# Performance work log

Hardware: AMD Instinct MI355X
Metric: run time of the kernel (lower is better)

Reference implementation:

```python
import jax, jax.numpy as jnp
import numpy as np

NUM_HEADS = 16
TOP_K = 2

def setup_inputs() -> dict:
    key = jax.random.key(0)
    ks = jax.random.split(key, 5)
    B, D, E = 8192, 2048, 8
    x = jax.random.normal(ks[0], (B, D), dtype=jnp.float32)
    W_qkv = jax.random.normal(ks[1], (E, D, 3 * D), dtype=jnp.float32) * 0.02  # (in,out) per expert
    W_gate = jax.random.normal(ks[2], (D, E), dtype=jnp.float32) * 0.02
    b_gate = jnp.zeros((E,), dtype=jnp.float32)
    W_proj = jax.random.normal(ks[3], (D, D), dtype=jnp.float32) * 0.02
    b_proj = jnp.zeros((D,), dtype=jnp.float32)
    return {"x": x, "W_qkv": W_qkv, "W_gate": W_gate, "b_gate": b_gate,
            "W_proj": W_proj, "b_proj": b_proj}


def reference(x, W_qkv, W_gate, b_gate, W_proj, b_proj):
    B, D = x.shape
    E = W_qkv.shape[0]
    H = NUM_HEADS
    hd = D // H
    scale = float(hd) ** -0.5

    # gating + top-k (sparse gate weights, zeros for non-selected experts)
    gate_scores = jax.nn.softmax(x @ W_gate + b_gate, axis=-1)        # (B, E)
    topk_vals, topk_idx = jax.lax.top_k(gate_scores, TOP_K)           # (B, K)
    gw = jnp.zeros_like(gate_scores).at[jnp.arange(B)[:, None], topk_idx].add(topk_vals)

    # gate-weighted combine of expert QKV projections (linear => combine after GEMM)
    qkv = jnp.zeros((B, 3 * D), dtype=x.dtype)
    for e in range(E):  # fixed small expert count; each iter is one big GEMM
        qkv = qkv + gw[:, e:e + 1] * (x @ W_qkv[e])
    qkv = qkv.reshape(B, 3, H, hd)

    # NOTE: the torch source writes `q = k = v = torch.zeros(...)` then uses
    # in-place `+=`, so q, k, v ALIAS one tensor: all equal gate*(q_i+k_i+v_i).
    # We replicate that exact math faithfully.
    s = qkv.sum(axis=1)                                               # (B, H, hd)

    attn = jax.nn.softmax(jnp.einsum('bhd,bgd->bhg', s, s) * scale, axis=-1)  # (B, H, H)
    out = jnp.einsum('bhg,bgd->bhd', attn, s)                         # (B, H, hd)
    out = out.transpose(0, 2, 1).reshape(B, D)                        # matches .transpose(1,2).reshape
    return out @ W_proj + b_proj
```

## Files before the change

### kernel.cpp

```cpp
#include <hip/hip_runtime.h>

#define B_ROWS 8192
#define DDIM 2048
#define NEXP 8
#define NASSIGN (B_ROWS * 2)
#define MAX_TILES 80

typedef unsigned short u16;
typedef short bf16x8 __attribute__((ext_vector_type(8)));
typedef float f32x4 __attribute__((ext_vector_type(4)));

#define M_CNT 0
#define M_FILL 8
#define M_SEG 16
#define M_TE 32
#define M_TB 112
#define M_TR 192

__device__ __forceinline__ u16 f2b(float f) {
  union { float f; unsigned u; } c; c.f = f;
  return (u16)((c.u + 0x7fffu + ((c.u >> 16) & 1u)) >> 16);
}
__device__ __forceinline__ float b2f(u16 h) {
  union { unsigned u; float f; } c; c.u = ((unsigned)h) << 16;
  return c.f;
}
__device__ __forceinline__ void async16(u16* lds, const u16* g) {
  __builtin_amdgcn_global_load_lds(
      (const __attribute__((address_space(1))) unsigned int*)g,
      (__attribute__((address_space(3))) unsigned int*)lds, 16, 0, 0);
}

__global__ void init_meta_kernel(int* meta) {
  int t = threadIdx.x;
  if (t < 32) meta[t] = 0;
}

template <int NSUM>
__global__ __launch_bounds__(256) void prep_transpose(
    const float* __restrict__ Win, u16* __restrict__ Wout, int ldin) {
  __shared__ u16 tl[64][72];
  int bx = blockIdx.x;
  int nt = bx & 31, kt = (bx >> 5) & 31, e = bx >> 10;
  int t = threadIdx.x;
  const size_t in_base = (size_t)e * DDIM * (size_t)ldin;
  int k0 = kt * 64, n0 = nt * 64;
#pragma unroll
  for (int i = 0; i < 4; ++i) {
    int idx = i * 256 + t;
    int kl = idx >> 4, f4 = idx & 15;
    const float* p = Win + in_base + (size_t)(k0 + kl) * ldin + n0 + f4 * 4;
    float4 v = *(const float4*)p;
    if (NSUM == 3) {
      float4 v1 = *(const float4*)(p + 2048);
      float4 v2 = *(const float4*)(p + 4096);
      v.x += v1.x + v2.x; v.y += v1.y + v2.y;
      v.z += v1.z + v2.z; v.w += v1.w + v2.w;
    }
    tl[f4 * 4 + 0][kl] = f2b(v.x);
    tl[f4 * 4 + 1][kl] = f2b(v.y);
    tl[f4 * 4 + 2][kl] = f2b(v.z);
    tl[f4 * 4 + 3][kl] = f2b(v.w);
  }
  __syncthreads();
  u16* out = Wout + (size_t)e * DDIM * DDIM;
#pragma unroll
  for (int i = 0; i < 2; ++i) {
    int idx = i * 256 + t;
    int nl = idx >> 3, kc = idx & 7;
    const u16* r = &tl[nl][kc * 8];
    uint4 pk;
    pk.x = (unsigned)r[0] | ((unsigned)r[1] << 16);
    pk.y = (unsigned)r[2] | ((unsigned)r[3] << 16);
    pk.z = (unsigned)r[4] | ((unsigned)r[5] << 16);
    pk.w = (unsigned)r[6] | ((unsigned)r[7] << 16);
    *(uint4*)(out + (size_t)(n0 + nl) * DDIM + k0 + kc * 8) = pk;
  }
}

__global__ __launch_bounds__(256) void gate_kernel(
    const float* __restrict__ x, const float* __restrict__ Wg,
    const float* __restrict__ bg, u16* __restrict__ xb,
    int* __restrict__ e01, float* __restrict__ w01, int* __restrict__ meta) {
  int b = blockIdx.x, t = threadIdx.x;
  const float* xr = x + (size_t)b * DDIM;
  float4 v0 = ((const float4*)xr)[2 * t];
  float4 v1 = ((const float4*)xr)[2 * t + 1];
  float xv[8] = {v0.x, v0.y, v0.z, v0.w, v1.x, v1.y, v1.z, v1.w};
  uint4 pk;
  pk.x = (unsigned)f2b(xv[0]) | ((unsigned)f2b(xv[1]) << 16);
  pk.y = (unsigned)f2b(xv[2]) | ((unsigned)f2b(xv[3]) << 16);
  pk.z = (unsigned)f2b(xv[4]) | ((unsigned)f2b(xv[5]) << 16);
  pk.w = (unsigned)f2b(xv[6]) | ((unsigned)f2b(xv[7]) << 16);
  *(uint4*)(xb + (size_t)b * DDIM + t * 8) = pk;

  double acc[8] = {0, 0, 0, 0, 0, 0, 0, 0};
#pragma unroll
  for (int j = 0; j < 8; ++j) {
    const float4* wr = (const float4*)(Wg + (size_t)(t * 8 + j) * 8);
    float4 wa = wr[0], wb = wr[1];
    double xd = (double)xv[j];
    acc[0] += xd * wa.x; acc[1] += xd * wa.y;
    acc[2] += xd * wa.z; acc[3] += xd * wa.w;
    acc[4] += xd * wb.x; acc[5] += xd * wb.y;
    acc[6] += xd * wb.z; acc[7] += xd * wb.w;
  }
#pragma unroll
  for (int e = 0; e < 8; ++e)
    for (int m2 = 32; m2; m2 >>= 1) acc[e] += __shfl_xor(acc[e], m2);
  __shared__ double red[4][8];
  if ((t & 63) == 0)
    for (int e = 0; e < 8; ++e) red[t >> 6][e] = acc[e];
  __syncthreads();
  if (t == 0) {
    double l[8];
    for (int e = 0; e < 8; ++e)
      l[e] = red[0][e] + red[1][e] + red[2][e] + red[3][e] + (double)bg[e];
    double mx = l[0];
    for (int e = 1; e < 8; ++e) mx = l[e] > mx ? l[e] : mx;
    double p[8], s = 0;
    for (int e = 0; e < 8; ++e) { p[e] = exp(l[e] - mx); s += p[e]; }
    int i1 = 0;
    for (int e = 1; e < 8; ++e) if (p[e] > p[i1]) i1 = e;
    int i2 = (i1 == 0) ? 1 : 0;
    for (int e = 0; e < 8; ++e)
      if (e != i1 && p[e] > p[i2]) i2 = e;
    e01[2 * b] = i1; e01[2 * b + 1] = i2;
    w01[2 * b] = (float)(p[i1] / s);
    w01[2 * b + 1] = (float)(p[i2] / s);
    atomicAdd(&meta[M_CNT + i1], 1);
    atomicAdd(&meta[M_CNT + i2], 1);
  }
}

__global__ __launch_bounds__(128) void scan_kernel(int* meta) {
  __shared__ int scnt[8];
  int t = threadIdx.x;
  if (t < 8) scnt[t] = meta[M_CNT + t];
  __syncthreads();
  int seg[9], pre[9];
  seg[0] = 0; pre[0] = 0;
#pragma unroll
  for (int e = 0; e < 8; ++e) {
    seg[e + 1] = seg[e] + scnt[e];
    pre[e + 1] = pre[e] + ((scnt[e] + 255) >> 8);
  }
  if (t < 8) meta[M_SEG + t] = seg[t];
  if (t < MAX_TILES) {
    if (t < pre[8]) {
      int e = 0;
      while (e < 7 && t >= pre[e + 1]) ++e;
      int i = t - pre[e];
      meta[M_TE + t] = e;
      meta[M_TB + t] = seg[e] + i * 256;
      meta[M_TR + t] = scnt[e] - i * 256;
    } else {
      meta[M_TE + t] = 0; meta[M_TB + t] = 0; meta[M_TR + t] = 0;
    }
  }
}

__global__ __launch_bounds__(256) void build_kernel(
    const int* __restrict__ e01, const float* __restrict__ w01,
    int* __restrict__ meta, int* __restrict__ rows, float* __restrict__ wt,
    int* __restrict__ rowpos) {
  int b = blockIdx.x * 256 + threadIdx.x;
  if (b >= B_ROWS) return;
#pragma unroll
  for (int s = 0; s < 2; ++s) {
    int e = e01[2 * b + s];
    float w = w01[2 * b + s];
    int p = meta[M_SEG + e] + atomicAdd(&meta[M_FILL + e], 1);
    rows[p] = b;
    wt[p] = w;
    rowpos[2 * b + s] = p;
  }
}

#define BAR()                           \
  do {                                  \
    __builtin_amdgcn_sched_barrier(0);  \
    __builtin_amdgcn_s_barrier();       \
    __builtin_amdgcn_sched_barrier(0);  \
  } while (0)
#define VMCNT2() asm volatile("s_waitcnt vmcnt(2)" ::: "memory")
#define VMCNT0() asm volatile("s_waitcnt vmcnt(0)" ::: "memory")
#define LGKM0()                                       \
  do {                                                \
    asm volatile("s_waitcnt lgkmcnt(0)" ::: "memory"); \
    __builtin_amdgcn_sched_barrier(0);                \
  } while (0)

#define STAGE_A(L, T, BB) async16(&lds[BB][0][(L)*4096 + t * 8], srcA[L] + (size_t)(T)*64)
#define STAGE_B(L, T, BB) async16(&lds[BB][1][(L)*4096 + t * 8], srcB[L] + (size_t)(T)*64)

#define READ_A(QM)                                                   \
  do {                                                               \
    _Pragma("unroll") for (int i_ = 0; i_ < 4; ++i_) {               \
      int rb_ = baseA + ((QM)*64 + i_ * 16) * 128;                   \
      af[i_][0] = *(const bf16x8*)(pA + rb_ + ck0);                  \
      af[i_][1] = *(const bf16x8*)(pA + rb_ + ck1);                  \
    }                                                                \
  } while (0)
#define READ_B(H)                                                    \
  do {                                                               \
    _Pragma("unroll") for (int j_ = 0; j_ < 2; ++j_) {               \
      int rb_ = baseB + (((H)*2 + j_) * 16) * 128;                   \
      bfr[(H)*2 + j_][0] = *(const bf16x8*)(pB + rb_ + ck0);         \
      bfr[(H)*2 + j_][1] = *(const bf16x8*)(pB + rb_ + ck1);         \
    }                                                                \
  } while (0)
#define MFMA16(QM, QN)                                                         \
  do {                                                                         \
    _Pragma("unroll") for (int i_ = 0; i_ < 4; ++i_) {                         \
      _Pragma("unroll") for (int j_ = 0; j_ < 2; ++j_) {                       \
        acc[(QM)*4 + i_][(QN)*2 + j_] = __builtin_amdgcn_mfma_f32_16x16x32_bf16( \
            af[i_][0], bfr[(QN)*2 + j_][0], acc[(QM)*4 + i_][(QN)*2 + j_], 0, 0, 0); \
        acc[(QM)*4 + i_][(QN)*2 + j_] = __builtin_amdgcn_mfma_f32_16x16x32_bf16( \
            af[i_][1], bfr[(QN)*2 + j_][1], acc[(QM)*4 + i_][(QN)*2 + j_], 0, 0, 0); \
      }                                                                        \
    }                                                                          \
  } while (0)

template <int MODE>
__global__ __launch_bounds__(512, 2) void gemm256_kernel(
    const u16* __restrict__ A, const u16* __restrict__ BT,
    const int* __restrict__ meta, const int* __restrict__ rows,
    const float* __restrict__ wt, const float* __restrict__ bias,
    u16* __restrict__ Yc, float* __restrict__ Out) {
  __shared__ __align__(16) u16 lds[2][2][16384];

  int e = 0, base = 0, rem = 256, m0 = 0;
  if (MODE == 0) {
    rem = meta[M_TR + blockIdx.y];
    if (rem <= 0) return;
    if (rem > 256) rem = 256;
    e = meta[M_TE + blockIdx.y];
    base = meta[M_TB + blockIdx.y];
  } else {
    m0 = blockIdx.y * 256;
  }
  const int n0 = blockIdx.x * 256;
  const int t = threadIdx.x;
  const int lane = t & 63;
  const int wid = t >> 6;
  const int wr = wid >> 2, wc = wid & 3;
  const int l15 = lane & 15;
  const int kg = lane >> 4;
  const int sw = lane & 7;

  const u16* srcA[4];
  const u16* srcB[4];
#pragma unroll
  for (int L = 0; L < 4; ++L) {
    int row = L * 64 + (t >> 3);
    int cl = (t & 7) ^ (row & 7);
    int grow;
    if (MODE == 0) {
      int rl = row < rem ? row : 0;
      grow = rows[base + rl];
    } else {
      grow = m0 + row;
    }
    srcA[L] = A + (size_t)grow * DDIM + cl * 8;
    srcB[L] = BT + ((size_t)e * DDIM + n0 + row) * DDIM + cl * 8;
  }

  f32x4 acc[8][4];
#pragma unroll
  for (int i = 0; i < 8; ++i)
#pragma unroll
    for (int j = 0; j < 4; ++j) {
      f32x4 z = {0.f, 0.f, 0.f, 0.f};
      acc[i][j] = z;
    }

  const int baseA = (wr * 128 + l15) * 128;
  const int baseB = (wc * 64 + l15) * 128;
  const int ck0 = ((0 * 4 + kg) ^ sw) << 4;
  const int ck1 = ((1 * 4 + kg) ^ sw) << 4;

  bf16x8 af[4][2];
  bf16x8 bfr[4][2];

  STAGE_A(0, 0, 0); STAGE_A(1, 0, 0); STAGE_A(2, 0, 0); STAGE_A(3, 0, 0);
  STAGE_B(0, 0, 0); STAGE_B(1, 0, 0); STAGE_B(2, 0, 0); STAGE_B(3, 0, 0);
  STAGE_A(0, 1, 1); STAGE_A(1, 1, 1);
  VMCNT2();
  BAR();

  const int NT = DDIM / 64;
  for (int T = 0; T < NT; ++T) {
    const int cb = T & 1, nb = cb ^ 1;
    const char* pA = (const char*)&lds[cb][0][0];
    const char* pB = (const char*)&lds[cb][1][0];
    READ_A(0);
    READ_B(0);
    if (T + 1 < NT) { STAGE_A(2, T + 1, nb); STAGE_A(3, T + 1, nb); }
    BAR();
    LGKM0();
    __builtin_amdgcn_s_setprio(1);
    MFMA16(0, 0);
    __builtin_amdgcn_s_setprio(0);
    BAR();
    READ_B(1);
    if (T + 1 < NT) { STAGE_B(0, T + 1, nb); STAGE_B(1, T + 1, nb); }
    BAR();
    LGKM0();
    __builtin_amdgcn_s_setprio(1);
    MFMA16(0, 1);
    __builtin_amdgcn_s_setprio(0);
    BAR();
    READ_A(1);
    if (T + 1 < NT) { STAGE_B(2, T + 1, nb); STAGE_B(3, T + 1, nb); }
    BAR();
    LGKM0();
    __builtin_amdgcn_s_setprio(1);
    MFMA16(1, 0);
    __builtin_amdgcn_s_setprio(0);
    BAR();
    if (T + 2 < NT) {
      STAGE_A(0, T + 2, cb); STAGE_A(1, T + 2, cb);
      VMCNT2();
    } else {
      VMCNT0();
    }
    BAR();
    __builtin_amdgcn_s_setprio(1);
    MFMA16(1, 1);
    __builtin_amdgcn_s_setprio(0);
    BAR();
  }

  if (MODE == 1) {
    float bv[4];
#pragma unroll
    for (int fn = 0; fn < 4; ++fn) bv[fn] = bias[n0 + wc * 64 + fn * 16 + l15];
#pragma unroll
    for (int qm = 0; qm < 2; ++qm)
#pragma unroll
      for (int i = 0; i < 4; ++i)
#pragma unroll
        for (int r = 0; r < 4; ++r) {
          int rl = wr * 128 + qm * 64 + i * 16 + kg * 4 + r;
          float* orow = Out + (size_t)(m0 + rl) * DDIM + n0 + wc * 64 + l15;
#pragma unroll
          for (int fn = 0; fn < 4; ++fn)
            orow[fn * 16] = acc[qm * 4 + i][fn][r] + bv[fn];
        }
  } else {
#pragma unroll
    for (int qm = 0; qm < 2; ++qm)
#pragma unroll
      for (int i = 0; i < 4; ++i)
#pragma unroll
        for (int r = 0; r < 4; ++r) {
          int rl = wr * 128 + qm * 64 + i * 16 + kg * 4 + r;
          if (rl < rem) {
            int pos = base + rl;
            float w = wt[pos];
            u16* yrow = Yc + (size_t)pos * DDIM + n0 + wc * 64 + l15;
#pragma unroll
            for (int fn = 0; fn < 4; ++fn)
              yrow[fn * 16] = f2b(w * acc[qm * 4 + i][fn][r]);
          }
        }
  }
}

__global__ __launch_bounds__(64) void combine_attn_kernel(
    const u16* __restrict__ Yc, const int* __restrict__ rowpos,
    u16* __restrict__ ab) {
  __shared__ __align__(16) u16 sb[16][136];
  __shared__ __align__(16) u16 pl[16][20];
  const int b = blockIdx.x, l = threadIdx.x;
  const int p0 = rowpos[2 * b], p1 = rowpos[2 * b + 1];
  const uint4* r0 = (const uint4*)(Yc + (size_t)p0 * DDIM + l * 32);
  const uint4* r1 = (const uint4*)(Yc + (size_t)p1 * DDIM + l * 32);
  {
    const int h = l >> 2, cbase = (l & 3) * 32;
#pragma unroll
    for (int q = 0; q < 4; ++q) {
      uint4 a = r0[q], c = r1[q];
      const unsigned* au = (const unsigned*)&a;
      const unsigned* cu = (const unsigned*)&c;
      uint4 w;
      unsigned* wu = (unsigned*)&w;
#pragma unroll
      for (int j = 0; j < 4; ++j) {
        float lo = b2f((u16)(au[j] & 0xffff)) + b2f((u16)(cu[j] & 0xffff));
        float hi = b2f((u16)(au[j] >> 16)) + b2f((u16)(cu[j] >> 16));
        wu[j] = (unsigned)f2b(lo) | ((unsigned)f2b(hi) << 16);
      }
      *(uint4*)&sb[h][cbase + q * 8] = w;
    }
  }
  __syncthreads();
  const int hh = l & 15, kg = l >> 4;
  f32x4 S = {0.f, 0.f, 0.f, 0.f};
#pragma unroll
  for (int kc = 0; kc < 4; ++kc) {
    bf16x8 f = *(const bf16x8*)&sb[hh][kc * 32 + kg * 8];
    S = __builtin_amdgcn_mfma_f32_16x16x32_bf16(f, f, S, 0, 0, 0);
  }
  const float sc = 0.088388347648318447f;
  float lg[4];
  float mx = -1e30f;
#pragma unroll
  for (int r = 0; r < 4; ++r) { lg[r] = S[r] * sc; mx = fmaxf(mx, lg[r]); }
  mx = fmaxf(mx, __shfl_xor(mx, 16));
  mx = fmaxf(mx, __shfl_xor(mx, 32));
  float p[4], sum = 0.f;
#pragma unroll
  for (int r = 0; r < 4; ++r) { p[r] = expf(lg[r] - mx); sum += p[r]; }
  sum += __shfl_xor(sum, 16);
  sum += __shfl_xor(sum, 32);
  const float inv = 1.f / sum;
#pragma unroll
  for (int r = 0; r < 4; ++r) pl[hh][kg * 4 + r] = f2b(p[r] * inv);
  __syncthreads();
  bf16x8 pa = {0, 0, 0, 0, 0, 0, 0, 0};
  if (kg < 2) pa = *(const bf16x8*)&pl[hh][kg * 8];
  u16* orow = ab + (size_t)b * DDIM;
#pragma unroll
  for (int c = 0; c < 8; ++c) {
    bf16x8 bv = {0, 0, 0, 0, 0, 0, 0, 0};
    if (kg < 2) {
      u16* bvp = (u16*)&bv;
#pragma unroll
      for (int j = 0; j < 8; ++j) bvp[j] = sb[kg * 8 + j][c * 16 + hh];
    }
    f32x4 z = {0.f, 0.f, 0.f, 0.f};
    f32x4 o = __builtin_amdgcn_mfma_f32_16x16x32_bf16(pa, bv, z, 0, 0, 0);
    uint2 st;
    st.x = (unsigned)f2b(o[0]) | ((unsigned)f2b(o[1]) << 16);
    st.y = (unsigned)f2b(o[2]) | ((unsigned)f2b(o[3]) << 16);
    *(uint2*)(orow + (c * 16 + hh) * 16 + kg * 4) = st;
  }
}

extern "C" void kernel_launch(void* const* d_in, const int* in_sizes, int n_in,
                              void* d_out, int out_size, void* d_ws, size_t ws_size,
                              hipStream_t stream) {
  const float* x = (const float*)d_in[0];
  const float* Wqkv = (const float*)d_in[1];
  const float* Wg = (const float*)d_in[2];
  const float* bg = (const float*)d_in[3];
  const float* Wp = (const float*)d_in[4];
  const float* bp = (const float*)d_in[5];
  float* out = (float*)d_out;

  char* ws = (char*)d_ws;
  size_t off = 0;
  auto alloc = [&](size_t bytes) {
    void* p = ws + off;
    off += (bytes + 255) & ~(size_t)255;
    return p;
  };
  u16* xb = (u16*)alloc((size_t)B_ROWS * DDIM * 2);
  u16* WsumT = (u16*)alloc((size_t)NEXP * DDIM * DDIM * 2);
  u16* WprojT = (u16*)alloc((size_t)DDIM * DDIM * 2);
  u16* Yc = (u16*)alloc((size_t)NASSIGN * DDIM * 2);
  u16* ab = (u16*)alloc((size_t)B_ROWS * DDIM * 2);
  int* e01 = (int*)alloc((size_t)NASSIGN * 4);
  float* w01 = (float*)alloc((size_t)NASSIGN * 4);
  int* rows = (int*)alloc((size_t)NASSIGN * 4);
  float* wt = (float*)alloc((size_t)NASSIGN * 4);
  int* rowpos = (int*)alloc((size_t)NASSIGN * 4);
  int* meta = (int*)alloc(4096);

  init_meta_kernel<<<dim3(1), dim3(64), 0, stream>>>(meta);
  prep_transpose<3><<<dim3(NEXP * 32 * 32), dim3(256), 0, stream>>>(Wqkv, WsumT, 3 * DDIM);
  prep_transpose<1><<<dim3(32 * 32), dim3(256), 0, stream>>>(Wp, WprojT, DDIM);
  gate_kernel<<<dim3(B_ROWS), dim3(256), 0, stream>>>(x, Wg, bg, xb, e01, w01, meta);
  scan_kernel<<<dim3(1), dim3(128), 0, stream>>>(meta);
  build_kernel<<<dim3(32), dim3(256), 0, stream>>>(e01, w01, meta, rows, wt, rowpos);
  gemm256_kernel<0><<<dim3(8, MAX_TILES), dim3(512), 0, stream>>>(
      xb, WsumT, meta, rows, wt, nullptr, Yc, nullptr);
  combine_attn_kernel<<<dim3(B_ROWS), dim3(64), 0, stream>>>(Yc, rowpos, ab);
  gemm256_kernel<1><<<dim3(8, 32), dim3(512), 0, stream>>>(
      ab, WprojT, meta, rows, wt, bp, nullptr, out);
  (void)in_sizes; (void)n_in; (void)out_size; (void)ws_size;
}
```

Baseline: 673.3 us.

## Use 128-row expert GEMM tiles with swizzled grid and fuse prologue kernels

```diff
diff --git a/kernel.cpp b/kernel.cpp
--- a/kernel.cpp
+++ b/kernel.cpp
@@ -4,7 +4,7 @@
 #define DDIM 2048
 #define NEXP 8
 #define NASSIGN (B_ROWS * 2)
-#define MAX_TILES 80
+#define MAX_TILES 136
 
 typedef unsigned short u16;
 typedef short bf16x8 __attribute__((ext_vector_type(8)));
@@ -13,9 +13,9 @@
 #define M_CNT 0
 #define M_FILL 8
 #define M_SEG 16
-#define M_TE 32
-#define M_TB 112
-#define M_TR 192
+#define M_TE 48
+#define M_TB 184
+#define M_TR 320
 
 __device__ __forceinline__ u16 f2b(float f) {
   union { float f; unsigned u; } c; c.f = f;
@@ -36,53 +36,61 @@
   if (t < 32) meta[t] = 0;
 }
 
-template <int NSUM>
-__global__ __launch_bounds__(256) void prep_transpose(
-    const float* __restrict__ Win, u16* __restrict__ Wout, int ldin) {
+__global__ __launch_bounds__(256) void prologue_kernel(
+    const float* __restrict__ x, const float* __restrict__ Wqkv,
+    const float* __restrict__ Wg, const float* __restrict__ bg,
+    const float* __restrict__ Wp, u16* __restrict__ xb,
+    u16* __restrict__ WsumT, u16* __restrict__ WprojT,
+    int* __restrict__ e01, float* __restrict__ w01, int* __restrict__ meta) {
   __shared__ u16 tl[64][72];
-  int bx = blockIdx.x;
-  int nt = bx & 31, kt = (bx >> 5) & 31, e = bx >> 10;
-  int t = threadIdx.x;
-  const size_t in_base = (size_t)e * DDIM * (size_t)ldin;
-  int k0 = kt * 64, n0 = nt * 64;
-#pragma unroll
-  for (int i = 0; i < 4; ++i) {
-    int idx = i * 256 + t;
-    int kl = idx >> 4, f4 = idx & 15;
-    const float* p = Win + in_base + (size_t)(k0 + kl) * ldin + n0 + f4 * 4;
-    float4 v = *(const float4*)p;
-    if (NSUM == 3) {
-      float4 v1 = *(const float4*)(p + 2048);
-      float4 v2 = *(const float4*)(p + 4096);
-      v.x += v1.x + v2.x; v.y += v1.y + v2.y;
-      v.z += v1.z + v2.z; v.w += v1.w + v2.w;
-    }
-    tl[f4 * 4 + 0][kl] = f2b(v.x);
-    tl[f4 * 4 + 1][kl] = f2b(v.y);
-    tl[f4 * 4 + 2][kl] = f2b(v.z);
-    tl[f4 * 4 + 3][kl] = f2b(v.w);
-  }
-  __syncthreads();
-  u16* out = Wout + (size_t)e * DDIM * DDIM;
-#pragma unroll
-  for (int i = 0; i < 2; ++i) {
-    int idx = i * 256 + t;
-    int nl = idx >> 3, kc = idx & 7;
-    const u16* r = &tl[nl][kc * 8];
-    uint4 pk;
-    pk.x = (unsigned)r[0] | ((unsigned)r[1] << 16);
-    pk.y = (unsigned)r[2] | ((unsigned)r[3] << 16);
-    pk.z = (unsigned)r[4] | ((unsigned)r[5] << 16);
-    pk.w = (unsigned)r[6] | ((unsigned)r[7] << 16);
-    *(uint4*)(out + (size_t)(n0 + nl) * DDIM + k0 + kc * 8) = pk;
-  }
-}
-
-__global__ __launch_bounds__(256) void gate_kernel(
-    const float* __restrict__ x, const float* __restrict__ Wg,
-    const float* __restrict__ bg, u16* __restrict__ xb,
-    int* __restrict__ e01, float* __restrict__ w01, int* __restrict__ meta) {
-  int b = blockIdx.x, t = threadIdx.x;
+  __shared__ double red[4][8];
+  const int bid = blockIdx.x;
+  const int t = threadIdx.x;
+
+  if (bid < 9216) {
+    const float* Win;
+    u16* Wout;
+    int ldin, nsum, bx;
+    if (bid < 8192) { Win = Wqkv; Wout = WsumT; ldin = 3 * DDIM; nsum = 3; bx = bid; }
+    else            { Win = Wp;   Wout = WprojT; ldin = DDIM;    nsum = 1; bx = bid - 8192; }
+    int nt = bx & 31, kt = (bx >> 5) & 31, e = bx >> 10;
+    const size_t in_base = (size_t)e * DDIM * (size_t)ldin;
+    int k0 = kt * 64, n0 = nt * 64;
+#pragma unroll
+    for (int i = 0; i < 4; ++i) {
+      int idx = i * 256 + t;
+      int kl = idx >> 4, f4 = idx & 15;
+      const float* p = Win + in_base + (size_t)(k0 + kl) * ldin + n0 + f4 * 4;
+      float4 v = *(const float4*)p;
+      if (nsum == 3) {
+        float4 v1 = *(const float4*)(p + 2048);
+        float4 v2 = *(const float4*)(p + 4096);
+        v.x += v1.x + v2.x; v.y += v1.y + v2.y;
+        v.z += v1.z + v2.z; v.w += v1.w + v2.w;
+      }
+      tl[f4 * 4 + 0][kl] = f2b(v.x);
+      tl[f4 * 4 + 1][kl] = f2b(v.y);
+      tl[f4 * 4 + 2][kl] = f2b(v.z);
+      tl[f4 * 4 + 3][kl] = f2b(v.w);
+    }
+    __syncthreads();
+    u16* out = Wout + (size_t)e * DDIM * DDIM;
+#pragma unroll
+    for (int i = 0; i < 2; ++i) {
+      int idx = i * 256 + t;
+      int nl = idx >> 3, kc = idx & 7;
+      const u16* r = &tl[nl][kc * 8];
+      uint4 pk;
+      pk.x = (unsigned)r[0] | ((unsigned)r[1] << 16);
+      pk.y = (unsigned)r[2] | ((unsigned)r[3] << 16);
+      pk.z = (unsigned)r[4] | ((unsigned)r[5] << 16);
+      pk.w = (unsigned)r[6] | ((unsigned)r[7] << 16);
+      *(uint4*)(out + (size_t)(n0 + nl) * DDIM + k0 + kc * 8) = pk;
+    }
+    return;
+  }
+
+  const int b = bid - 9216;
   const float* xr = x + (size_t)b * DDIM;
   float4 v0 = ((const float4*)xr)[2 * t];
   float4 v1 = ((const float4*)xr)[2 * t + 1];
@@ -108,7 +116,6 @@
 #pragma unroll
   for (int e = 0; e < 8; ++e)
     for (int m2 = 32; m2; m2 >>= 1) acc[e] += __shfl_xor(acc[e], m2);
-  __shared__ double red[4][8];
   if ((t & 63) == 0)
     for (int e = 0; e < 8; ++e) red[t >> 6][e] = acc[e];
   __syncthreads();
@@ -133,7 +140,7 @@
   }
 }
 
-__global__ __launch_bounds__(128) void scan_kernel(int* meta) {
+__global__ __launch_bounds__(256) void scan_kernel(int* meta) {
   __shared__ int scnt[8];
   int t = threadIdx.x;
   if (t < 8) scnt[t] = meta[M_CNT + t];
@@ -143,7 +150,7 @@
 #pragma unroll
   for (int e = 0; e < 8; ++e) {
     seg[e + 1] = seg[e] + scnt[e];
-    pre[e + 1] = pre[e] + ((scnt[e] + 255) >> 8);
+    pre[e + 1] = pre[e] + ((scnt[e] + 127) >> 7);
   }
   if (t < 8) meta[M_SEG + t] = seg[t];
   if (t < MAX_TILES) {
@@ -152,8 +159,8 @@
       while (e < 7 && t >= pre[e + 1]) ++e;
       int i = t - pre[e];
       meta[M_TE + t] = e;
-      meta[M_TB + t] = seg[e] + i * 256;
-      meta[M_TR + t] = scnt[e] - i * 256;
+      meta[M_TB + t] = seg[e] + i * 128;
+      meta[M_TR + t] = scnt[e] - i * 128;
     } else {
       meta[M_TE + t] = 0; meta[M_TB + t] = 0; meta[M_TR + t] = 0;
     }
@@ -191,9 +198,148 @@
     __builtin_amdgcn_sched_barrier(0);                \
   } while (0)
 
+__global__ __launch_bounds__(512, 1) void gemm_exp_kernel(
+    const u16* __restrict__ A, const u16* __restrict__ BT,
+    const int* __restrict__ meta, const int* __restrict__ rows,
+    const float* __restrict__ wt, u16* __restrict__ Yc) {
+  __shared__ __align__(16) u16 ldsA[2][8192];
+  __shared__ __align__(16) u16 ldsB[2][16384];
+
+  const int orig = blockIdx.x;
+  const int wgid = (orig & 7) * 136 + (orig >> 3);
+  const int mt = wgid >> 3;
+  const int n0 = (wgid & 7) << 8;
+
+  int rem = meta[M_TR + mt];
+  if (rem <= 0) return;
+  if (rem > 128) rem = 128;
+  const int e = meta[M_TE + mt];
+  const int base = meta[M_TB + mt];
+
+  const int t = threadIdx.x;
+  const int lane = t & 63;
+  const int wid = t >> 6;
+  const int wr = wid >> 2, wc = wid & 3;
+  const int l15 = lane & 15;
+  const int kg = lane >> 4;
+  const int sw = lane & 7;
+
+  const u16* srcA[2];
+  const u16* srcB[4];
+#pragma unroll
+  for (int L = 0; L < 4; ++L) {
+    int row = L * 64 + (t >> 3);
+    int cl = (t & 7) ^ (row & 7);
+    if (L < 2) {
+      int rl = (L * 64 + (t >> 3)) < rem ? (L * 64 + (t >> 3)) : 0;
+      srcA[L] = A + (size_t)rows[base + rl] * DDIM + cl * 8;
+    }
+    srcB[L] = BT + ((size_t)e * DDIM + n0 + row) * DDIM + cl * 8;
+  }
+
+  f32x4 acc[4][4];
+#pragma unroll
+  for (int i = 0; i < 4; ++i)
+#pragma unroll
+    for (int j = 0; j < 4; ++j) {
+      f32x4 z = {0.f, 0.f, 0.f, 0.f};
+      acc[i][j] = z;
+    }
+
+  const int baseA = (wr * 64 + l15) * 128;
+  const int baseB = (wc * 64 + l15) * 128;
+  const int ck0 = ((0 * 4 + kg) ^ sw) << 4;
+  const int ck1 = ((1 * 4 + kg) ^ sw) << 4;
+
+  bf16x8 af[4][2];
+  bf16x8 bfr[4][2];
+
+#define ESTAGE_A(L, T, BB) async16(&ldsA[BB][(L)*4096 + t * 8], srcA[L] + (size_t)(T)*64)
+#define ESTAGE_B(L, T, BB) async16(&ldsB[BB][(L)*4096 + t * 8], srcB[L] + (size_t)(T)*64)
+#define EREAD_A()                                                    \
+  do {                                                               \
+    _Pragma("unroll") for (int i_ = 0; i_ < 4; ++i_) {               \
+      int rb_ = baseA + (i_ * 16) * 128;                             \
+      af[i_][0] = *(const bf16x8*)(pA + rb_ + ck0);                  \
+      af[i_][1] = *(const bf16x8*)(pA + rb_ + ck1);                  \
+    }                                                                \
+  } while (0)
+#define EREAD_B(H)                                                   \
+  do {                                                               \
+    _Pragma("unroll") for (int j_ = 0; j_ < 2; ++j_) {               \
+      int rb_ = baseB + (((H)*2 + j_) * 16) * 128;                   \
+      bfr[(H)*2 + j_][0] = *(const bf16x8*)(pB + rb_ + ck0);         \
+      bfr[(H)*2 + j_][1] = *(const bf16x8*)(pB + rb_ + ck1);         \
+    }                                                                \
+  } while (0)
+#define EMFMA(QN)                                                              \
+  do {                                                                         \
+    _Pragma("unroll") for (int i_ = 0; i_ < 4; ++i_) {                         \
+      _Pragma("unroll") for (int j_ = 0; j_ < 2; ++j_) {                       \
+        acc[i_][(QN)*2 + j_] = __builtin_amdgcn_mfma_f32_16x16x32_bf16(        \
+            af[i_][0], bfr[(QN)*2 + j_][0], acc[i_][(QN)*2 + j_], 0, 0, 0);    \
+        acc[i_][(QN)*2 + j_] = __builtin_amdgcn_mfma_f32_16x16x32_bf16(        \
+            af[i_][1], bfr[(QN)*2 + j_][1], acc[i_][(QN)*2 + j_], 0, 0, 0);    \
+      }                                                                        \
+    }                                                                          \
+  } while (0)
+
+  ESTAGE_B(0, 0, 0); ESTAGE_B(1, 0, 0); ESTAGE_B(2, 0, 0); ESTAGE_B(3, 0, 0);
+  ESTAGE_A(0, 0, 0); ESTAGE_A(1, 0, 0);
+  ESTAGE_A(0, 1, 1); ESTAGE_A(1, 1, 1);
+  VMCNT2();
+  BAR();
+
+  const int NT = DDIM / 64;
+  for (int T = 0; T < NT; ++T) {
+    const int cb = T & 1, nb = cb ^ 1;
+    const char* pA = (const char*)&ldsA[cb][0];
+    const char* pB = (const char*)&ldsB[cb][0];
+    EREAD_A();
+    EREAD_B(0);
+    if (T + 1 < NT) {
+      ESTAGE_B(0, T + 1, nb); ESTAGE_B(1, T + 1, nb);
+      ESTAGE_B(2, T + 1, nb); ESTAGE_B(3, T + 1, nb);
+    }
+    BAR();
+    LGKM0();
+    __builtin_amdgcn_s_setprio(1);
+    EMFMA(0);
+    __builtin_amdgcn_s_setprio(0);
+    BAR();
+    EREAD_B(1);
+    if (T + 2 < NT) {
+      ESTAGE_A(0, T + 2, cb); ESTAGE_A(1, T + 2, cb);
+      VMCNT2();
+    } else {
+      VMCNT0();
+    }
+    BAR();
+    LGKM0();
+    __builtin_amdgcn_s_setprio(1);
+    EMFMA(1);
+    __builtin_amdgcn_s_setprio(0);
+    BAR();
+  }
+
+#pragma unroll
+  for (int i = 0; i < 4; ++i)
+#pragma unroll
+    for (int r = 0; r < 4; ++r) {
+      int rl = wr * 64 + i * 16 + kg * 4 + r;
+      if (rl < rem) {
+        int pos = base + rl;
+        float w2 = wt[pos];
+        u16* yrow = Yc + (size_t)pos * DDIM + n0 + wc * 64 + l15;
+#pragma unroll
+        for (int fn = 0; fn < 4; ++fn)
+          yrow[fn * 16] = f2b(w2 * acc[i][fn][r]);
+      }
+    }
+}
+
 #define STAGE_A(L, T, BB) async16(&lds[BB][0][(L)*4096 + t * 8], srcA[L] + (size_t)(T)*64)
 #define STAGE_B(L, T, BB) async16(&lds[BB][1][(L)*4096 + t * 8], srcB[L] + (size_t)(T)*64)
-
 #define READ_A(QM)                                                   \
   do {                                                               \
     _Pragma("unroll") for (int i_ = 0; i_ < 4; ++i_) {               \
@@ -222,24 +368,12 @@
     }                                                                          \
   } while (0)
 
-template <int MODE>
-__global__ __launch_bounds__(512, 2) void gemm256_kernel(
+__global__ __launch_bounds__(512, 2) void gemm_proj_kernel(
     const u16* __restrict__ A, const u16* __restrict__ BT,
-    const int* __restrict__ meta, const int* __restrict__ rows,
-    const float* __restrict__ wt, const float* __restrict__ bias,
-    u16* __restrict__ Yc, float* __restrict__ Out) {
+    const float* __restrict__ bias, float* __restrict__ Out) {
   __shared__ __align__(16) u16 lds[2][2][16384];
 
-  int e = 0, base = 0, rem = 256, m0 = 0;
-  if (MODE == 0) {
-    rem = meta[M_TR + blockIdx.y];
-    if (rem <= 0) return;
-    if (rem > 256) rem = 256;
-    e = meta[M_TE + blockIdx.y];
-    base = meta[M_TB + blockIdx.y];
-  } else {
-    m0 = blockIdx.y * 256;
-  }
+  const int m0 = blockIdx.y * 256;
   const int n0 = blockIdx.x * 256;
   const int t = threadIdx.x;
   const int lane = t & 63;
@@ -255,15 +389,8 @@
   for (int L = 0; L < 4; ++L) {
     int row = L * 64 + (t >> 3);
     int cl = (t & 7) ^ (row & 7);
-    int grow;
-    if (MODE == 0) {
-      int rl = row < rem ? row : 0;
-      grow = rows[base + rl];
-    } else {
-      grow = m0 + row;
-    }
-    srcA[L] = A + (size_t)grow * DDIM + cl * 8;
-    srcB[L] = BT + ((size_t)e * DDIM + n0 + row) * DDIM + cl * 8;
+    srcA[L] = A + (size_t)(m0 + row) * DDIM + cl * 8;
+    srcB[L] = BT + (size_t)(n0 + row) * DDIM + cl * 8;
   }
 
   f32x4 acc[8][4];
@@ -332,40 +459,21 @@
     BAR();
   }
 
-  if (MODE == 1) {
-    float bv[4];
-#pragma unroll
-    for (int fn = 0; fn < 4; ++fn) bv[fn] = bias[n0 + wc * 64 + fn * 16 + l15];
-#pragma unroll
-    for (int qm = 0; qm < 2; ++qm)
-#pragma unroll
-      for (int i = 0; i < 4; ++i)
-#pragma unroll
-        for (int r = 0; r < 4; ++r) {
-          int rl = wr * 128 + qm * 64 + i * 16 + kg * 4 + r;
-          float* orow = Out + (size_t)(m0 + rl) * DDIM + n0 + wc * 64 + l15;
-#pragma unroll
-          for (int fn = 0; fn < 4; ++fn)
-            orow[fn * 16] = acc[qm * 4 + i][fn][r] + bv[fn];
-        }
-  } else {
-#pragma unroll
-    for (int qm = 0; qm < 2; ++qm)
-#pragma unroll
-      for (int i = 0; i < 4; ++i)
-#pragma unroll
-        for (int r = 0; r < 4; ++r) {
-          int rl = wr * 128 + qm * 64 + i * 16 + kg * 4 + r;
-          if (rl < rem) {
-            int pos = base + rl;
-            float w = wt[pos];
-            u16* yrow = Yc + (size_t)pos * DDIM + n0 + wc * 64 + l15;
-#pragma unroll
-            for (int fn = 0; fn < 4; ++fn)
-              yrow[fn * 16] = f2b(w * acc[qm * 4 + i][fn][r]);
-          }
-        }
-  }
+  float bv[4];
+#pragma unroll
+  for (int fn = 0; fn < 4; ++fn) bv[fn] = bias[n0 + wc * 64 + fn * 16 + l15];
+#pragma unroll
+  for (int qm = 0; qm < 2; ++qm)
+#pragma unroll
+    for (int i = 0; i < 4; ++i)
+#pragma unroll
+      for (int r = 0; r < 4; ++r) {
+        int rl = wr * 128 + qm * 64 + i * 16 + kg * 4 + r;
+        float* orow = Out + (size_t)(m0 + rl) * DDIM + n0 + wc * 64 + l15;
+#pragma unroll
+        for (int fn = 0; fn < 4; ++fn)
+          orow[fn * 16] = acc[qm * 4 + i][fn][r] + bv[fn];
+      }
 }
 
 __global__ __launch_bounds__(64) void combine_attn_kernel(
@@ -470,15 +578,13 @@
   int* meta = (int*)alloc(4096);
 
   init_meta_kernel<<<dim3(1), dim3(64), 0, stream>>>(meta);
-  prep_transpose<3><<<dim3(NEXP * 32 * 32), dim3(256), 0, stream>>>(Wqkv, WsumT, 3 * DDIM);
-  prep_transpose<1><<<dim3(32 * 32), dim3(256), 0, stream>>>(Wp, WprojT, DDIM);
-  gate_kernel<<<dim3(B_ROWS), dim3(256), 0, stream>>>(x, Wg, bg, xb, e01, w01, meta);
-  scan_kernel<<<dim3(1), dim3(128), 0, stream>>>(meta);
+  prologue_kernel<<<dim3(17408), dim3(256), 0, stream>>>(
+      x, Wqkv, Wg, bg, Wp, xb, WsumT, WprojT, e01, w01, meta);
+  scan_kernel<<<dim3(1), dim3(256), 0, stream>>>(meta);
   build_kernel<<<dim3(32), dim3(256), 0, stream>>>(e01, w01, meta, rows, wt, rowpos);
-  gemm256_kernel<0><<<dim3(8, MAX_TILES), dim3(512), 0, stream>>>(
-      xb, WsumT, meta, rows, wt, nullptr, Yc, nullptr);
+  gemm_exp_kernel<<<dim3(8 * MAX_TILES), dim3(512), 0, stream>>>(
+      xb, WsumT, meta, rows, wt, Yc);
   combine_attn_kernel<<<dim3(B_ROWS), dim3(64), 0, stream>>>(Yc, rowpos, ab);
-  gemm256_kernel<1><<<dim3(8, 32), dim3(512), 0, stream>>>(
-      ab, WprojT, meta, rows, wt, bp, nullptr, out);
+  gemm_proj_kernel<<<dim3(8, 32), dim3(512), 0, stream>>>(ab, WprojT, bp, out);
   (void)in_sizes; (void)n_in; (void)out_size; (void)ws_size;
 }
```

New measurement: 707.8 us. 5.1% more time.

## Split weight prep into streaming sum-convert pass and bf16 tiled transpose

Applied to the files above, without the earlier changes.

```diff
diff --git a/kernel.cpp b/kernel.cpp
--- a/kernel.cpp
+++ b/kernel.cpp
@@ -36,45 +36,90 @@
   if (t < 32) meta[t] = 0;
 }
 
-template <int NSUM>
-__global__ __launch_bounds__(256) void prep_transpose(
-    const float* __restrict__ Win, u16* __restrict__ Wout, int ldin) {
-  __shared__ u16 tl[64][72];
-  int bx = blockIdx.x;
-  int nt = bx & 31, kt = (bx >> 5) & 31, e = bx >> 10;
-  int t = threadIdx.x;
-  const size_t in_base = (size_t)e * DDIM * (size_t)ldin;
-  int k0 = kt * 64, n0 = nt * 64;
-#pragma unroll
-  for (int i = 0; i < 4; ++i) {
+__global__ __launch_bounds__(256) void sumcvt_kernel(
+    const float* __restrict__ Wqkv, const float* __restrict__ Wp,
+    u16* __restrict__ Wsum, u16* __restrict__ WprojN) {
+  const long long NV_E = (long long)NEXP * 2048 * 256;
+  const long long NV_P = 2048 * 256;
+  long long v = (long long)blockIdx.x * 256 + threadIdx.x;
+  const long long stride = (long long)gridDim.x * 256;
+  for (; v < NV_E + NV_P; v += stride) {
+    float s[8];
+    u16* dst;
+    if (v < NV_E) {
+      int e = (int)(v >> 19);
+      int rem = (int)(v & 524287);
+      int k = rem >> 8, nc = rem & 255;
+      const float* p = Wqkv + (size_t)e * 2048 * 6144 + (size_t)k * 6144 + nc * 8;
+      float4 a0 = *(const float4*)p, a1 = *(const float4*)(p + 4);
+      float4 b0 = *(const float4*)(p + 2048), b1 = *(const float4*)(p + 2052);
+      float4 c0 = *(const float4*)(p + 4096), c1 = *(const float4*)(p + 4100);
+      s[0] = a0.x + b0.x + c0.x; s[1] = a0.y + b0.y + c0.y;
+      s[2] = a0.z + b0.z + c0.z; s[3] = a0.w + b0.w + c0.w;
+      s[4] = a1.x + b1.x + c1.x; s[5] = a1.y + b1.y + c1.y;
+      s[6] = a1.z + b1.z + c1.z; s[7] = a1.w + b1.w + c1.w;
+      dst = Wsum + ((size_t)e * 2048 + k) * 2048 + nc * 8;
+    } else {
+      int rem = (int)(v - NV_E);
+      int k = rem >> 8, nc = rem & 255;
+      const float* p = Wp + (size_t)k * 2048 + nc * 8;
+      float4 a0 = *(const float4*)p, a1 = *(const float4*)(p + 4);
+      s[0] = a0.x; s[1] = a0.y; s[2] = a0.z; s[3] = a0.w;
+      s[4] = a1.x; s[5] = a1.y; s[6] = a1.z; s[7] = a1.w;
+      dst = WprojN + (size_t)k * 2048 + nc * 8;
+    }
+    uint4 pk;
+    pk.x = (unsigned)f2b(s[0]) | ((unsigned)f2b(s[1]) << 16);
+    pk.y = (unsigned)f2b(s[2]) | ((unsigned)f2b(s[3]) << 16);
+    pk.z = (unsigned)f2b(s[4]) | ((unsigned)f2b(s[5]) << 16);
+    pk.w = (unsigned)f2b(s[6]) | ((unsigned)f2b(s[7]) << 16);
+    *(uint4*)dst = pk;
+  }
+}
+
+__global__ __launch_bounds__(256) void transpose_kernel(
+    const u16* __restrict__ Wsum, const u16* __restrict__ WprojN,
+    u16* __restrict__ WsumT, u16* __restrict__ WprojT) {
+  __shared__ __align__(16) u16 tl[128][136];
+  const int orig = blockIdx.x;
+  const int bid = (orig & 7) * 288 + (orig >> 3);
+  const u16* src;
+  u16* dst;
+  int tk, tn;
+  if (bid < 2048) {
+    int e = bid >> 8, tile = bid & 255;
+    tk = tile >> 4; tn = tile & 15;
+    src = Wsum + (size_t)e * 2048 * 2048;
+    dst = WsumT + (size_t)e * 2048 * 2048;
+  } else {
+    int tile = bid - 2048;
+    tk = tile >> 4; tn = tile & 15;
+    src = WprojN;
+    dst = WprojT;
+  }
+  const int k0 = tk * 128, n0 = tn * 128;
+  const int t = threadIdx.x;
+#pragma unroll
+  for (int i = 0; i < 8; ++i) {
     int idx = i * 256 + t;
-    int kl = idx >> 4, f4 = idx & 15;
-    const float* p = Win + in_base + (size_t)(k0 + kl) * ldin + n0 + f4 * 4;
-    float4 v = *(const float4*)p;
-    if (NSUM == 3) {
-      float4 v1 = *(const float4*)(p + 2048);
-      float4 v2 = *(const float4*)(p + 4096);
-      v.x += v1.x + v2.x; v.y += v1.y + v2.y;
-      v.z += v1.z + v2.z; v.w += v1.w + v2.w;
-    }
-    tl[f4 * 4 + 0][kl] = f2b(v.x);
-    tl[f4 * 4 + 1][kl] = f2b(v.y);
-    tl[f4 * 4 + 2][kl] = f2b(v.z);
-    tl[f4 * 4 + 3][kl] = f2b(v.w);
+    int r = idx >> 4, c = idx & 15;
+    *(uint4*)&tl[r][c * 8] =
+        *(const uint4*)(src + (size_t)(k0 + r) * 2048 + n0 + c * 8);
   }
   __syncthreads();
-  u16* out = Wout + (size_t)e * DDIM * DDIM;
-#pragma unroll
-  for (int i = 0; i < 2; ++i) {
+#pragma unroll
+  for (int i = 0; i < 8; ++i) {
     int idx = i * 256 + t;
-    int nl = idx >> 3, kc = idx & 7;
-    const u16* r = &tl[nl][kc * 8];
+    int n = idx & 127, kc = idx >> 7;
+    u16 r8[8];
+#pragma unroll
+    for (int j = 0; j < 8; ++j) r8[j] = tl[kc * 8 + j][n];
     uint4 pk;
-    pk.x = (unsigned)r[0] | ((unsigned)r[1] << 16);
-    pk.y = (unsigned)r[2] | ((unsigned)r[3] << 16);
-    pk.z = (unsigned)r[4] | ((unsigned)r[5] << 16);
-    pk.w = (unsigned)r[6] | ((unsigned)r[7] << 16);
-    *(uint4*)(out + (size_t)(n0 + nl) * DDIM + k0 + kc * 8) = pk;
+    pk.x = (unsigned)r8[0] | ((unsigned)r8[1] << 16);
+    pk.y = (unsigned)r8[2] | ((unsigned)r8[3] << 16);
+    pk.z = (unsigned)r8[4] | ((unsigned)r8[5] << 16);
+    pk.w = (unsigned)r8[6] | ((unsigned)r8[7] << 16);
+    *(uint4*)(dst + (size_t)(n0 + n) * 2048 + k0 + kc * 8) = pk;
   }
 }
 
@@ -460,6 +505,8 @@
   u16* xb = (u16*)alloc((size_t)B_ROWS * DDIM * 2);
   u16* WsumT = (u16*)alloc((size_t)NEXP * DDIM * DDIM * 2);
   u16* WprojT = (u16*)alloc((size_t)DDIM * DDIM * 2);
+  u16* Wsum = (u16*)alloc((size_t)NEXP * DDIM * DDIM * 2);
+  u16* WprojN = (u16*)alloc((size_t)DDIM * DDIM * 2);
   u16* Yc = (u16*)alloc((size_t)NASSIGN * DDIM * 2);
   u16* ab = (u16*)alloc((size_t)B_ROWS * DDIM * 2);
   int* e01 = (int*)alloc((size_t)NASSIGN * 4);
@@ -470,11 +517,11 @@
   int* meta = (int*)alloc(4096);
 
   init_meta_kernel<<<dim3(1), dim3(64), 0, stream>>>(meta);
-  prep_transpose<3><<<dim3(NEXP * 32 * 32), dim3(256), 0, stream>>>(Wqkv, WsumT, 3 * DDIM);
-  prep_transpose<1><<<dim3(32 * 32), dim3(256), 0, stream>>>(Wp, WprojT, DDIM);
   gate_kernel<<<dim3(B_ROWS), dim3(256), 0, stream>>>(x, Wg, bg, xb, e01, w01, meta);
   scan_kernel<<<dim3(1), dim3(128), 0, stream>>>(meta);
   build_kernel<<<dim3(32), dim3(256), 0, stream>>>(e01, w01, meta, rows, wt, rowpos);
+  sumcvt_kernel<<<dim3(2048), dim3(256), 0, stream>>>(Wqkv, Wp, Wsum, WprojN);
+  transpose_kernel<<<dim3(2304), dim3(256), 0, stream>>>(Wsum, WprojN, WsumT, WprojT);
   gemm256_kernel<0><<<dim3(8, MAX_TILES), dim3(512), 0, stream>>>(
       xb, WsumT, meta, rows, wt, nullptr, Yc, nullptr);
   combine_attn_kernel<<<dim3(B_ROWS), dim3(64), 0, stream>>>(Yc, rowpos, ab);
```

New measurement: 710.9 us. 1.06x slower.
